# Performance work log

Measured on AMD Instinct MI355X. Metric: run time of the kernel, lower is better.

The kernel has to match this reference:

```python
import jax, jax.numpy as jnp
import numpy as np

L, N, H_IN, H = 512, 32, 1024, 1024


def _mk_params(key, in_dim, hid):
    ks = jax.random.split(key, 7)
    s_in = 1.0 / np.sqrt(in_dim)
    s_h = 1.0 / np.sqrt(hid)
    return dict(
        Wmx=jax.random.uniform(ks[0], (hid, in_dim), jnp.float32, -s_in, s_in),
        Wmh=jax.random.uniform(ks[1], (hid, hid), jnp.float32, -s_h, s_h),
        bmx=jax.random.uniform(ks[2], (hid,), jnp.float32, -s_in, s_in),
        bmh=jax.random.uniform(ks[3], (hid,), jnp.float32, -s_h, s_h),
        Wgx=jax.random.uniform(ks[4], (4 * hid, in_dim), jnp.float32, -s_in, s_in),
        Wgm=jax.random.uniform(ks[5], (4 * hid, hid), jnp.float32, -s_h, s_h),
        bg=jax.random.uniform(ks[6], (4 * hid,), jnp.float32, -s_h, s_h),
    )


def setup_inputs() -> dict:
    key = jax.random.key(0)
    k_in, k0, k1 = jax.random.split(key, 3)
    inp = {"inputs": jax.random.normal(k_in, (L, N, H_IN), jnp.float32)}
    for i, (k, d) in enumerate([(k0, H_IN), (k1, H)]):
        p = _mk_params(k, d, H)
        for name, v in p.items():
            inp[f"{name}{i}"] = v
    return inp


def _run_layer(xs, state, Wmx, Wmh, bmx, bmh, Wgx, Wgm, bg):
    # xs: (L, N, in_dim); state: ((N,H),(N,H))
    def step(carry, x_t):
        h, c = carry
        m = (x_t @ Wmx.T + bmx) * (h @ Wmh.T + bmh)  # multiplicative intermediate
        g = x_t @ Wgx.T + m @ Wgm.T + bg             # (N, 4H)
        i_g, f_g, z_g, o_g = jnp.split(g, 4, axis=-1)
        c_new = jax.nn.sigmoid(f_g) * c + jax.nn.sigmoid(i_g) * jnp.tanh(z_g)
        h_new = jax.nn.sigmoid(o_g) * jnp.tanh(c_new)
        return (h_new, c_new), h_new

    (h, c), ys = jax.lax.scan(step, state, xs)
    return ys, (h, c)


def reference(inputs, Wmx0, Wmh0, bmx0, bmh0, Wgx0, Wgm0, bg0,
              Wmx1, Wmh1, bmx1, bmh1, Wgx1, Wgm1, bg1):
    zeros = jnp.zeros((N, H), inputs.dtype)
    state = (zeros, zeros)
    # NOTE: original torch code carries hidden_state across layers (quirk kept).
    ys, state = _run_layer(inputs, state, Wmx0, Wmh0, bmx0, bmh0, Wgx0, Wgm0, bg0)
    hs, cs = [state[0]], [state[1]]
    ys, state = _run_layer(ys, state, Wmx1, Wmh1, bmx1, bmh1, Wgx1, Wgm1, bg1)
    hs.append(state[0]); cs.append(state[1])
    return ys, (jnp.stack(hs), jnp.stack(cs))
```

## Files before the change

### kernel.cpp

```cpp
#include <hip/hip_runtime.h>
#include <hip/hip_bf16.h>


typedef unsigned short u16;
typedef unsigned int u32;
typedef unsigned long long u64;
typedef __attribute__((ext_vector_type(8))) short bf16x8;
typedef __attribute__((ext_vector_type(4))) float f32x4;
typedef __attribute__((ext_vector_type(4))) unsigned int u32x4;

#define LSEQ 512
#define NB   32
#define HD   1024
#define G4   4096
#define YSZ  (LSEQ*NB*HD)
#define NH32 (NB*HD)
#define SEG  64
#define NSEG (LSEQ/SEG)
#define PERSIST_LDS 163840

#define ATOMIC_RLX __ATOMIC_RELAXED
#define SCOPE_AGT __HIP_MEMORY_SCOPE_AGENT

__device__ __forceinline__ float b2f(u16 u) {
    u32 i = ((u32)u) << 16; float f; __builtin_memcpy(&f, &i, 4); return f;
}
__device__ __forceinline__ u16 f2b(float f) {
    u32 x; __builtin_memcpy(&x, &f, 4);
    return (u16)((x + 0x7fffu + ((x >> 16) & 1u)) >> 16);
}
__device__ __forceinline__ int SW(int row, int byte) { return byte ^ ((row & 7) << 4); }

__device__ __forceinline__ void pollwait(const u32* flags, u32 target) {
    const int lane = threadIdx.x & 63;
    const u64* p = (const u64*)flags + (size_t)lane * 16;
    for (;;) {
        u64 v = __hip_atomic_load(p, ATOMIC_RLX, SCOPE_AGT);
        u32 lo = (u32)v, hi = (u32)(v >> 32);
        if (__all(lo >= target && hi >= target)) break;
        __builtin_amdgcn_s_sleep(1);
    }
    asm volatile("" ::: "memory");
}

__device__ __forceinline__ void load_row16(const char* base, u32x4* dst) {
#pragma unroll
    for (int kt = 0; kt < 32; ++kt) {
        u64 a = (u64)(base + kt * 64);
        asm volatile("global_load_dwordx4 %0, %1, off sc0 sc1"
                     : "=v"(dst[kt]) : "v"(a));
    }
    asm volatile("s_waitcnt vmcnt(0)" ::: "memory");
    __builtin_amdgcn_sched_barrier(0);
}

__device__ __forceinline__ void store_t16(u16* ebuf, int rowbase, int colbase,
                                          const u16 mu[4]) {
    const int d = threadIdx.x & 63;
    u32 wlo = (u32)mu[0] | ((u32)mu[1] << 16);
    u32 whi = (u32)mu[2] | ((u32)mu[3] << 16);
    const int Rl = d >> 1, half = d & 1;
    const int lks = Rl >> 2, r = Rl & 3;
    u32x4 outv;
#pragma unroll
    for (int p = 0; p < 4; ++p) {
        u32 v0, v1;
        {
            int s = lks * 16 + half * 8 + 2 * p;
            u32 a = (u32)__shfl((int)wlo, s);
            u32 bb = (u32)__shfl((int)whi, s);
            u32 pick = (r & 2) ? bb : a;
            v0 = (r & 1) ? (pick >> 16) : (pick & 0xFFFFu);
        }
        {
            int s = lks * 16 + half * 8 + 2 * p + 1;
            u32 a = (u32)__shfl((int)wlo, s);
            u32 bb = (u32)__shfl((int)whi, s);
            u32 pick = (r & 2) ? bb : a;
            v1 = (r & 1) ? (pick >> 16) : (pick & 0xFFFFu);
        }
        outv[p] = v0 | (v1 << 16);
    }
    if (d < 32) {
        u64 addr = (u64)ebuf + (size_t)(rowbase + Rl) * 2048 + colbase * 2 + half * 16;
        asm volatile("global_store_dwordx4 %0, %1, off sc0 sc1"
                     :: "v"(addr), "v"(outv) : "memory");
    }
}

__global__ void k_cvt(const float* __restrict__ s, u16* __restrict__ d, long n) {
    long i = (long)blockIdx.x * blockDim.x + threadIdx.x;
    long stride = (long)gridDim.x * blockDim.x;
    for (; i < n; i += stride) d[i] = f2b(s[i]);
}

template<typename XT> __device__ __forceinline__ bf16x8 ld8(const XT* p);
template<> __device__ __forceinline__ bf16x8 ld8<u16>(const u16* p) {
    return *(const bf16x8*)p;
}
template<> __device__ __forceinline__ bf16x8 ld8<float>(const float* p) {
    float4 a = *(const float4*)p, b = *(const float4*)(p + 4);
    bf16x8 r;
    r[0]=(short)f2b(a.x); r[1]=(short)f2b(a.y); r[2]=(short)f2b(a.z); r[3]=(short)f2b(a.w);
    r[4]=(short)f2b(b.x); r[5]=(short)f2b(b.y); r[6]=(short)f2b(b.z); r[7]=(short)f2b(b.w);
    return r;
}

template<typename XT>
__global__ __launch_bounds__(256) void k_gemm(
    const XT* __restrict__ X, const u16* __restrict__ W,
    const float* __restrict__ bias, u16* __restrict__ Out, int ldo)
{
    __shared__ u16 As[128][40];
    __shared__ u16 Bs[128][40];
    int bm = blockIdx.y, bn = blockIdx.x;
    int tid = threadIdx.x;
    int w = tid >> 6, lane = tid & 63;
    int wm = w >> 1, wn = w & 1;
    int l16 = lane & 15, lk = lane >> 4;

    f32x4 acc[4][4];
    #pragma unroll
    for (int i = 0; i < 4; ++i)
        #pragma unroll
        for (int j = 0; j < 4; ++j) acc[i][j] = (f32x4){0.f, 0.f, 0.f, 0.f};

    for (int kt = 0; kt < 32; ++kt) {
        __syncthreads();
        #pragma unroll
        for (int c = 0; c < 2; ++c) {
            int cid = tid + c * 256;
            int rrow = cid >> 2, kc = (cid & 3) * 8;
            *(bf16x8*)(&As[rrow][kc]) = ld8<XT>(X + (long)(bm * 128 + rrow) * HD + kt * 32 + kc);
            *(bf16x8*)(&Bs[rrow][kc]) = ld8<u16>(W + (long)(bn * 128 + rrow) * HD + kt * 32 + kc);
        }
        __syncthreads();
        bf16x8 af[4], bfr[4];
        #pragma unroll
        for (int mt = 0; mt < 4; ++mt)
            af[mt] = *(const bf16x8*)(&As[wm * 64 + mt * 16 + l16][lk * 8]);
        #pragma unroll
        for (int nt = 0; nt < 4; ++nt)
            bfr[nt] = *(const bf16x8*)(&Bs[wn * 64 + nt * 16 + l16][lk * 8]);
        #pragma unroll
        for (int mt = 0; mt < 4; ++mt)
            #pragma unroll
            for (int nt = 0; nt < 4; ++nt)
                acc[mt][nt] = __builtin_amdgcn_mfma_f32_16x16x32_bf16(
                    af[mt], bfr[nt], acc[mt][nt], 0, 0, 0);
    }
    #pragma unroll
    for (int mt = 0; mt < 4; ++mt)
        #pragma unroll
        for (int nt = 0; nt < 4; ++nt) {
            int colg = bn * 128 + wn * 64 + nt * 16 + l16;
            float bv = bias[colg];
            #pragma unroll
            for (int r = 0; r < 4; ++r) {
                int rowg = bm * 128 + wm * 64 + mt * 16 + lk * 4 + r;
                Out[(long)rowg * ldo + colg] = f2b(acc[mt][nt][r] + bv);
            }
        }
}

__global__ __launch_bounds__(256, 1) void k_persist(
    const u16* __restrict__ Wmhb, const float* __restrict__ bmh,
    const u16* __restrict__ Wgmb,
    const u16* __restrict__ Ab,
    const u16* __restrict__ Gxb,
    u16* eh, u16* em,
    float* __restrict__ cbuf,
    u16* __restrict__ yb, float* __restrict__ yf,
    float* __restrict__ tail,
    int l, int tbc, int tbi, u32* fM, u32* fH)
{
    extern __shared__ __align__(16) char lds[];
    const int tid = threadIdx.x;
    const int b = blockIdx.x;
    const int w = tid >> 6, lane = tid & 63;
    const int l16 = lane & 15, lk = lane >> 4;

    for (int it = 0; it < 32; ++it) {
        int cch = tid + it * 256;
        int lr = cch >> 7, k8 = cch & 127;
        int g = lr >> 4, c16 = lr & 15;
        bf16x8 v = *(const bf16x8*)(Wgmb + (long)(g * 1024 + 16 * b + c16) * HD + k8 * 8);
        *(bf16x8*)(lds + SW(lr, lr * 2048 + k8 * 16)) = v;
    }
    for (int it = 0; it < 8; ++it) {
        int cch = tid + it * 256;
        int lr = cch >> 7, k8 = cch & 127;
        bf16x8 v = *(const bf16x8*)(Wmhb + (long)(16 * b + lr) * HD + k8 * 8);
        *(bf16x8*)(lds + 131072 + SW(lr, lr * 2048 + k8 * 16)) = v;
    }
    __syncthreads();

    const int colg = 16 * b + l16;
    const int rt = w & 1;
    const bool isP1 = (w >= 2);

    const float bcol = bmh[colg];
    const char* hbase = (const char*)eh + (size_t)(rt * 16 + l16) * 2048 + lk * 16;
    const char* mbase = (const char*)em + (size_t)(rt * 16 + l16) * 2048 + lk * 16;
    f32x4 creg = (f32x4){0.f, 0.f, 0.f, 0.f};
    if (!isP1)
        #pragma unroll
        for (int r = 0; r < 4; ++r)
            creg[r] = cbuf[(rt * 16 + lk * 4 + r) * HD + colg];

    if (isP1) {
        for (int t = 0; t < SEG; ++t) {
            const u32 gt = (u32)(tbc + t);
            const u16* At = Ab + (long)(tbi + t) * NH32;
            u16 atv[4];
            #pragma unroll
            for (int r = 0; r < 4; ++r)
                atv[r] = At[(rt * 16 + lk * 4 + r) * HD + colg];
            pollwait(fH, gt);
            u32x4 hv[32];
            load_row16(hbase, hv);
            f32x4 acc = (f32x4){0.f, 0.f, 0.f, 0.f};
            #pragma unroll
            for (int kt = 0; kt < 32; ++kt) {
                union { u32x4 q; bf16x8 v; } u;
                u.q = hv[kt];
                bf16x8 bfrag = *(const bf16x8*)(lds + 131072 +
                                SW(l16, l16 * 2048 + kt * 64 + lk * 16));
                acc = __builtin_amdgcn_mfma_f32_16x16x32_bf16(u.v, bfrag, acc, 0, 0, 0);
            }
            u16 mu[4];
            #pragma unroll
            for (int r = 0; r < 4; ++r)
                mu[r] = f2b(b2f(atv[r]) * (acc[r] + bcol));
            store_t16(em, rt * 16, 16 * b, mu);
            asm volatile("s_waitcnt vmcnt(0)" ::: "memory");
            if (lane == 0)
                __hip_atomic_store(fM + b * 32 + rt, gt + 1, ATOMIC_RLX, SCOPE_AGT);
        }
    } else {
        for (int t = 0; t < SEG; ++t) {
            const u32 gt = (u32)(tbc + t);
            const u16* Gx = Gxb + (long)t * NB * G4;
            u16 gxv[4][4];
            #pragma unroll
            for (int g = 0; g < 4; ++g)
                #pragma unroll
                for (int r = 0; r < 4; ++r)
                    gxv[g][r] = Gx[(long)(rt * 16 + lk * 4 + r) * G4 + g * 1024 + colg];
            pollwait(fM, gt + 1);
            u32x4 mv[32];
            load_row16(mbase, mv);
            f32x4 gacc[4];
            #pragma unroll
            for (int g = 0; g < 4; ++g) gacc[g] = (f32x4){0.f, 0.f, 0.f, 0.f};
            #pragma unroll
            for (int kt = 0; kt < 32; ++kt) {
                union { u32x4 q; bf16x8 v; } u;
                u.q = mv[kt];
                #pragma unroll
                for (int g = 0; g < 4; ++g) {
                    int lr = g * 16 + l16;
                    bf16x8 bfrag = *(const bf16x8*)(lds + SW(lr, lr * 2048 + kt * 64 + lk * 16));
                    gacc[g] = __builtin_amdgcn_mfma_f32_16x16x32_bf16(u.v, bfrag, gacc[g], 0, 0, 0);
                }
            }
            float hn[4];
            u16 hu[4];
            #pragma unroll
            for (int r = 0; r < 4; ++r) {
                float ig = gacc[0][r] + b2f(gxv[0][r]);
                float fg = gacc[1][r] + b2f(gxv[1][r]);
                float zg = gacc[2][r] + b2f(gxv[2][r]);
                float og = gacc[3][r] + b2f(gxv[3][r]);
                float si = 1.f / (1.f + expf(-ig));
                float sf = 1.f / (1.f + expf(-fg));
                float so = 1.f / (1.f + expf(-og));
                float cn = sf * creg[r] + si * tanhf(zg);
                hn[r] = so * tanhf(cn);
                creg[r] = cn;
                hu[r] = f2b(hn[r]);
            }
            store_t16(eh, rt * 16, 16 * b, hu);
            asm volatile("s_waitcnt vmcnt(0)" ::: "memory");
            if (lane == 0)
                __hip_atomic_store(fH + b * 32 + rt, gt + 1, ATOMIC_RLX, SCOPE_AGT);
            #pragma unroll
            for (int r = 0; r < 4; ++r) {
                int row = rt * 16 + lk * 4 + r;
                long yidx = (long)(tbi + t) * NH32 + (long)row * HD + colg;
                if (yb) yb[yidx] = f2b(hn[r]); else yf[yidx] = hn[r];
                if (tbi + t == LSEQ - 1) {
                    tail[(long)l * NH32 + row * HD + colg] = hn[r];
                    tail[2L * NH32 + (long)l * NH32 + row * HD + colg] = creg[r];
                }
            }
        }
        #pragma unroll
        for (int r = 0; r < 4; ++r)
            cbuf[(rt * 16 + lk * 4 + r) * HD + colg] = creg[r];
    }
}

extern "C" void kernel_launch(void* const* d_in, const int* in_sizes, int n_in,
                              void* d_out, int out_size, void* d_ws, size_t ws_size,
                              hipStream_t stream) {
    (void)in_sizes; (void)n_in; (void)out_size; (void)ws_size;
    const float* inputs = (const float*)d_in[0];
    const float* Wmx[2] = {(const float*)d_in[1], (const float*)d_in[8]};
    const float* Wmh[2] = {(const float*)d_in[2], (const float*)d_in[9]};
    const float* bmx[2] = {(const float*)d_in[3], (const float*)d_in[10]};
    const float* bmh[2] = {(const float*)d_in[4], (const float*)d_in[11]};
    const float* Wgx[2] = {(const float*)d_in[5], (const float*)d_in[12]};
    const float* Wgm[2] = {(const float*)d_in[6], (const float*)d_in[13]};
    const float* bg[2]  = {(const float*)d_in[7], (const float*)d_in[14]};
    float* out = (float*)d_out;

    char* ws = (char*)d_ws;
    const long MB = 1024L * 1024L;
    u16* Wmxb[2] = {(u16*)(ws + 0 * MB),  (u16*)(ws + 2 * MB)};
    u16* Wmhb[2] = {(u16*)(ws + 4 * MB),  (u16*)(ws + 6 * MB)};
    u16* Wgxb[2] = {(u16*)(ws + 8 * MB),  (u16*)(ws + 16 * MB)};
    u16* Wgmb[2] = {(u16*)(ws + 24 * MB), (u16*)(ws + 32 * MB)};
    u16* Yb  = (u16*)(ws + 40 * MB);
    u16* Ab  = (u16*)(ws + 72 * MB);
    u16* Gxb = (u16*)(ws + 104 * MB);
    char* ex = ws + 120 * MB;
    u16* exch_h = (u16*)ex;
    u16* exch_m = (u16*)(ex + 65536);
    float* cbuf = (float*)(ex + 131072);
    u32* fM     = (u32*)(ex + 262144);
    u32* fH     = (u32*)(ex + 262144 + 8192);

    hipFuncSetAttribute((const void*)k_persist,
                        hipFuncAttributeMaxDynamicSharedMemorySize, PERSIST_LDS);

    hipMemsetAsync(ex, 0, 262144 + 16384, stream);

    k_cvt<<<512, 256, 0, stream>>>(Wmx[0], Wmxb[0], (long)HD * HD);
    k_cvt<<<512, 256, 0, stream>>>(Wmx[1], Wmxb[1], (long)HD * HD);
    k_cvt<<<512, 256, 0, stream>>>(Wmh[0], Wmhb[0], (long)HD * HD);
    k_cvt<<<512, 256, 0, stream>>>(Wmh[1], Wmhb[1], (long)HD * HD);
    k_cvt<<<1024, 256, 0, stream>>>(Wgx[0], Wgxb[0], (long)G4 * HD);
    k_cvt<<<1024, 256, 0, stream>>>(Wgx[1], Wgxb[1], (long)G4 * HD);
    k_cvt<<<1024, 256, 0, stream>>>(Wgm[0], Wgmb[0], (long)G4 * HD);
    k_cvt<<<1024, 256, 0, stream>>>(Wgm[1], Wgmb[1], (long)G4 * HD);

    for (int l = 0; l < 2; ++l) {
        if (l == 0)
            k_gemm<float><<<dim3(8, 128), 256, 0, stream>>>(inputs, Wmxb[0], bmx[0], Ab, HD);
        else
            k_gemm<u16><<<dim3(8, 128), 256, 0, stream>>>(Yb, Wmxb[1], bmx[1], Ab, HD);
        for (int s = 0; s < NSEG; ++s) {
            if (l == 0)
                k_gemm<float><<<dim3(32, 16), 256, 0, stream>>>(
                    inputs + (long)s * SEG * NB * HD, Wgxb[0], bg[0], Gxb, G4);
            else
                k_gemm<u16><<<dim3(32, 16), 256, 0, stream>>>(
                    Yb + (long)s * SEG * NB * HD, Wgxb[1], bg[1], Gxb, G4);
            k_persist<<<64, 256, PERSIST_LDS, stream>>>(
                Wmhb[l], bmh[l], Wgmb[l], Ab, Gxb,
                exch_h, exch_m, cbuf,
                l ? nullptr : Yb, l ? out : nullptr, out + YSZ,
                l, l * LSEQ + s * SEG, s * SEG, fM, fH);
        }
    }
}
```

Measured before the change: 14.80 ms.

## Replace flag polling with parity bits embedded in exchanged bf16 data

Removes the separate flag arrays, the flag polling and the store-wait-then-flag-publish sequence between the producer and consumer wave groups. Each exchanged bf16 value now carries a step-parity bit in its LSB, and readers reload the whole row until every element shows the expected parity. This drops one global round trip and a vmcnt drain per timestep on the recurrence critical path. In exchange it loses one mantissa bit of precision in h and m, and it relies on each 16-byte store landing atomically so a row can never mix old and new data.

```diff
diff --git a/kernel.cpp b/kernel.cpp
--- a/kernel.cpp
+++ b/kernel.cpp
@@ -31,26 +31,24 @@
 }
 __device__ __forceinline__ int SW(int row, int byte) { return byte ^ ((row & 7) << 4); }
 
-__device__ __forceinline__ void pollwait(const u32* flags, u32 target) {
-    const int lane = threadIdx.x & 63;
-    const u64* p = (const u64*)flags + (size_t)lane * 16;
+__device__ __forceinline__ void load_rowv(const char* base, u32x4* dst, u32 expw) {
     for (;;) {
-        u64 v = __hip_atomic_load(p, ATOMIC_RLX, SCOPE_AGT);
-        u32 lo = (u32)v, hi = (u32)(v >> 32);
-        if (__all(lo >= target && hi >= target)) break;
-        __builtin_amdgcn_s_sleep(1);
-    }
-    asm volatile("" ::: "memory");
-}
-
-__device__ __forceinline__ void load_row16(const char* base, u32x4* dst) {
 #pragma unroll
-    for (int kt = 0; kt < 32; ++kt) {
-        u64 a = (u64)(base + kt * 64);
-        asm volatile("global_load_dwordx4 %0, %1, off sc0 sc1"
-                     : "=v"(dst[kt]) : "v"(a));
-    }
-    asm volatile("s_waitcnt vmcnt(0)" ::: "memory");
+        for (int kt = 0; kt < 32; ++kt) {
+            u64 a = (u64)(base + kt * 64);
+            asm volatile("global_load_dwordx4 %0, %1, off sc0 sc1"
+                         : "=v"(dst[kt]) : "v"(a));
+        }
+        asm volatile("s_waitcnt vmcnt(0)" ::: "memory");
+        u32 bad = 0;
+#pragma unroll
+        for (int kt = 0; kt < 32; ++kt)
+#pragma unroll
+            for (int p = 0; p < 4; ++p)
+                bad |= (dst[kt][p] ^ expw) & 0x00010001u;
+        if (__all(bad == 0)) break;
+        __builtin_amdgcn_s_sleep(2);
+    }
     __builtin_amdgcn_sched_barrier(0);
 }
 
@@ -88,6 +86,10 @@
     }
 }
 
+__global__ void k_fill(u32* __restrict__ d, int n, u32 v) {
+    int i = blockIdx.x * blockDim.x + threadIdx.x;
+    if (i < n) d[i] = v;
+}
 __global__ void k_cvt(const float* __restrict__ s, u16* __restrict__ d, long n) {
     long i = (long)blockIdx.x * blockDim.x + threadIdx.x;
     long stride = (long)gridDim.x * blockDim.x;
@@ -172,7 +174,7 @@
     float* __restrict__ cbuf,
     u16* __restrict__ yb, float* __restrict__ yf,
     float* __restrict__ tail,
-    int l, int tbc, int tbi, u32* fM, u32* fH)
+    int l, int tbc, int tbi)
 {
     extern __shared__ __align__(16) char lds[];
     const int tid = threadIdx.x;
@@ -211,14 +213,15 @@
     if (isP1) {
         for (int t = 0; t < SEG; ++t) {
             const u32 gt = (u32)(tbc + t);
+            const u32 expw_h = ((gt + 1) & 1u) ? 0x00010001u : 0u;
+            const u16 pm = (u16)(gt & 1u);
             const u16* At = Ab + (long)(tbi + t) * NH32;
             u16 atv[4];
             #pragma unroll
             for (int r = 0; r < 4; ++r)
                 atv[r] = At[(rt * 16 + lk * 4 + r) * HD + colg];
-            pollwait(fH, gt);
             u32x4 hv[32];
-            load_row16(hbase, hv);
+            load_rowv(hbase, hv, expw_h);
             f32x4 acc = (f32x4){0.f, 0.f, 0.f, 0.f};
             #pragma unroll
             for (int kt = 0; kt < 32; ++kt) {
@@ -231,15 +234,14 @@
             u16 mu[4];
             #pragma unroll
             for (int r = 0; r < 4; ++r)
-                mu[r] = f2b(b2f(atv[r]) * (acc[r] + bcol));
+                mu[r] = (u16)((f2b(b2f(atv[r]) * (acc[r] + bcol)) & 0xFFFEu) | pm);
             store_t16(em, rt * 16, 16 * b, mu);
-            asm volatile("s_waitcnt vmcnt(0)" ::: "memory");
-            if (lane == 0)
-                __hip_atomic_store(fM + b * 32 + rt, gt + 1, ATOMIC_RLX, SCOPE_AGT);
         }
     } else {
         for (int t = 0; t < SEG; ++t) {
             const u32 gt = (u32)(tbc + t);
+            const u32 expw_m = (gt & 1u) ? 0x00010001u : 0u;
+            const u16 pm = (u16)(gt & 1u);
             const u16* Gx = Gxb + (long)t * NB * G4;
             u16 gxv[4][4];
             #pragma unroll
@@ -247,9 +249,8 @@
                 #pragma unroll
                 for (int r = 0; r < 4; ++r)
                     gxv[g][r] = Gx[(long)(rt * 16 + lk * 4 + r) * G4 + g * 1024 + colg];
-            pollwait(fM, gt + 1);
             u32x4 mv[32];
-            load_row16(mbase, mv);
+            load_rowv(mbase, mv, expw_m);
             f32x4 gacc[4];
             #pragma unroll
             for (int g = 0; g < 4; ++g) gacc[g] = (f32x4){0.f, 0.f, 0.f, 0.f};
@@ -278,12 +279,9 @@
                 float cn = sf * creg[r] + si * tanhf(zg);
                 hn[r] = so * tanhf(cn);
                 creg[r] = cn;
-                hu[r] = f2b(hn[r]);
+                hu[r] = (u16)((f2b(hn[r]) & 0xFFFEu) | pm);
             }
             store_t16(eh, rt * 16, 16 * b, hu);
-            asm volatile("s_waitcnt vmcnt(0)" ::: "memory");
-            if (lane == 0)
-                __hip_atomic_store(fH + b * 32 + rt, gt + 1, ATOMIC_RLX, SCOPE_AGT);
             #pragma unroll
             for (int r = 0; r < 4; ++r) {
                 int row = rt * 16 + lk * 4 + r;
@@ -328,13 +326,12 @@
     u16* exch_h = (u16*)ex;
     u16* exch_m = (u16*)(ex + 65536);
     float* cbuf = (float*)(ex + 131072);
-    u32* fM     = (u32*)(ex + 262144);
-    u32* fH     = (u32*)(ex + 262144 + 8192);
 
     hipFuncSetAttribute((const void*)k_persist,
                         hipFuncAttributeMaxDynamicSharedMemorySize, PERSIST_LDS);
 
-    hipMemsetAsync(ex, 0, 262144 + 16384, stream);
+    k_fill<<<128, 256, 0, stream>>>((u32*)ex, 32768, 0x00010001u);
+    hipMemsetAsync(cbuf, 0, 131072, stream);
 
     k_cvt<<<512, 256, 0, stream>>>(Wmx[0], Wmxb[0], (long)HD * HD);
     k_cvt<<<512, 256, 0, stream>>>(Wmx[1], Wmxb[1], (long)HD * HD);
@@ -361,7 +358,7 @@
                 Wmhb[l], bmh[l], Wgmb[l], Ab, Gxb,
                 exch_h, exch_m, cbuf,
                 l ? nullptr : Yb, l ? out : nullptr, out + YSZ,
-                l, l * LSEQ + s * SEG, s * SEG, fM, fH);
-        }
-    }
-}
+                l, l * LSEQ + s * SEG, s * SEG);
+        }
+    }
+}
```

Measured after the change: 31.19 ms. 111% more time.
